# Kernel optimization log

Hardware: AMD Instinct MI355X
Metric: run time of the kernel (lower is better)

Reference implementation:

```python
import jax, jax.numpy as jnp
import numpy as np

N_NODES = 50000
N_EDGES = 400000
D_IN = 512
DIM_H = 256
N_GRAPHS = 64
BN_EPS = 1e-5


def _linear_init(key, din, dout):
    kw, kb = jax.random.split(key)
    s = 1.0 / np.sqrt(din)
    W = jax.random.uniform(kw, (din, dout), jnp.float32, -s, s)
    b = jax.random.uniform(kb, (dout,), jnp.float32, -s, s)
    return W, b


def setup_inputs() -> dict:
    key = jax.random.key(0)
    ks = iter(jax.random.split(key, 64))
    inp = {}
    inp["x"] = jax.random.normal(next(ks), (N_NODES, D_IN), jnp.float32)
    inp["edge_index"] = jax.random.randint(next(ks), (2, N_EDGES), 0, N_NODES, jnp.int32)
    inp["batch"] = jnp.sort(jax.random.randint(next(ks), (N_NODES,), 0, N_GRAPHS, jnp.int32))
    dins = [D_IN, DIM_H, DIM_H]
    for l in range(3):
        p = "c%d_" % (l + 1)
        inp[p + "W1"], inp[p + "b1"] = _linear_init(next(ks), dins[l], DIM_H)
        inp[p + "gamma"] = jax.random.uniform(next(ks), (DIM_H,), jnp.float32, 0.5, 1.5)
        inp[p + "beta"] = 0.1 * jax.random.normal(next(ks), (DIM_H,), jnp.float32)
        inp[p + "mean"] = 0.1 * jax.random.normal(next(ks), (DIM_H,), jnp.float32)
        inp[p + "var"] = jax.random.uniform(next(ks), (DIM_H,), jnp.float32, 0.5, 1.5)
        inp[p + "W2"], inp[p + "b2"] = _linear_init(next(ks), DIM_H, DIM_H)
    inp["lin1_W"], inp["lin1_b"] = _linear_init(next(ks), 3 * DIM_H, 64)
    inp["lin2_W"], inp["lin2_b"] = _linear_init(next(ks), 64, 2)
    return inp


def _gin_layer(x, src, dst, W1, b1, gamma, beta, mean, var, W2, b2):
    # GINConv with eps=0: h_i = MLP(x_i + sum_{j->i} x_j); scatter-add over edges
    agg = jax.ops.segment_sum(x[src], dst, num_segments=x.shape[0])
    h = (x + agg) @ W1 + b1
    # eval-mode BatchNorm1d
    h = jax.nn.relu((h - mean) * jax.lax.rsqrt(var + BN_EPS) * gamma + beta)
    return jax.nn.relu(h @ W2 + b2)


def reference(x, edge_index, batch,
              c1_W1, c1_b1, c1_gamma, c1_beta, c1_mean, c1_var, c1_W2, c1_b2,
              c2_W1, c2_b1, c2_gamma, c2_beta, c2_mean, c2_var, c2_W2, c2_b2,
              c3_W1, c3_b1, c3_gamma, c3_beta, c3_mean, c3_var, c3_W2, c3_b2,
              lin1_W, lin1_b, lin2_W, lin2_b):
    src, dst = edge_index[0], edge_index[1]
    h1 = _gin_layer(x, src, dst, c1_W1, c1_b1, c1_gamma, c1_beta, c1_mean, c1_var, c1_W2, c1_b2)
    h2 = _gin_layer(h1, src, dst, c2_W1, c2_b1, c2_gamma, c2_beta, c2_mean, c2_var, c2_W2, c2_b2)
    h3 = _gin_layer(h2, src, dst, c3_W1, c3_b1, c3_gamma, c3_beta, c3_mean, c3_var, c3_W2, c3_b2)
    # global_add_pool per graph
    p1 = jax.ops.segment_sum(h1, batch, num_segments=N_GRAPHS)
    p2 = jax.ops.segment_sum(h2, batch, num_segments=N_GRAPHS)
    p3 = jax.ops.segment_sum(h3, batch, num_segments=N_GRAPHS)
    h = jnp.concatenate([p1, p2, p3], axis=1)
    h = jax.nn.relu(h @ lin1_W + lin1_b)
    # Dropout(p=0.8) is identity in eval mode
    h = h @ lin2_W + lin2_b
    return (h, jax.nn.log_softmax(h, axis=1))
```

## Files before the change

kernel.cpp:

```cpp
#include <hip/hip_runtime.h>
#include <hip/hip_bf16.h>

#define DIV_UP(a,b) (((a)+(b)-1)/(b))

static const int NN  = 50000;
static const int NE  = 400000;
static const int DIN = 512;
static const int DH  = 256;
static const int NG  = 64;
static const int MAXDEG = 64;

typedef unsigned short u16;
typedef unsigned int   u32;
typedef __attribute__((ext_vector_type(8))) short bf16x8;
typedef __attribute__((ext_vector_type(4))) float f32x4;

#define AS1(p) ((const __attribute__((address_space(1))) void*)(p))
#define AS3(p) ((__attribute__((address_space(3))) void*)(p))

__device__ inline u16 f2bf(float f) {
  u32 u = __float_as_uint(f);
  u += 0x7fffu + ((u >> 16) & 1u);
  return (u16)(u >> 16);
}
__device__ inline float bf2f(u16 h) { return __uint_as_float(((u32)h) << 16); }
__device__ inline void unpack2(u32 u, float& lo, float& hi) {
  lo = __uint_as_float(u << 16);
  hi = __uint_as_float(u & 0xffff0000u);
}
__device__ inline u32 pack2(float lo, float hi) {
  return (u32)f2bf(lo) | ((u32)f2bf(hi) << 16);
}

struct SetupArgs {
  const float* Wsrc[6]; u16* Wdst[6];
  const float* bn[15];
  float* scsh;
  int* cnt; float* PL;
};
static const int NB_W = (131072 + 5 * 65536) / 256;
static const int NB_Z = DIV_UP(NN + NG * 768, 256);

__global__ __launch_bounds__(256) void k_setup(SetupArgs a) {
  int b = blockIdx.x;
  if (b < NB_W) {
    int idx = b * 256 + threadIdx.x;
    if (idx < 131072) {
      int n = idx >> 9, k = idx & 511;
      a.Wdst[0][idx] = f2bf(a.Wsrc[0][(size_t)k * 256 + n]);
    } else {
      int r = idx - 131072;
      int s = 1 + (r >> 16);
      int ri = r & 65535;
      int n = ri >> 8, k = ri & 255;
      a.Wdst[s][ri] = f2bf(a.Wsrc[s][(size_t)k * 256 + n]);
    }
  } else if (b < NB_W + 3) {
    int l = b - NB_W, ch = threadIdx.x;
    float sc = rsqrtf(a.bn[l * 5 + 4][ch] + 1e-5f) * a.bn[l * 5 + 1][ch];
    float sh = (a.bn[l * 5 + 0][ch] - a.bn[l * 5 + 3][ch]) * sc + a.bn[l * 5 + 2][ch];
    a.scsh[l * 512 + ch] = sc;
    a.scsh[l * 512 + 256 + ch] = sh;
  } else {
    int i = (b - NB_W - 3) * 256 + threadIdx.x;
    if (i < NN) a.cnt[i] = 0;
    else if (i - NN < NG * 768) a.PL[i - NN] = 0.f;
  }
}

__global__ __launch_bounds__(256) void k_fill2(const int* __restrict__ src,
                                               const int* __restrict__ dst,
                                               int* __restrict__ cnt,
                                               int* __restrict__ adj, int nE) {
  int e = blockIdx.x * 256 + threadIdx.x;
  if (e >= nE) return;
  int d = dst[e];
  int pos = atomicAdd(&cnt[d], 1);
  if (pos < MAXDEG) adj[(size_t)d * MAXDEG + pos] = src[e];
}

__global__ __launch_bounds__(256) void k_gather_bn(const u16* __restrict__ Y,
                                                   const int* __restrict__ cnt,
                                                   const int* __restrict__ adj,
                                                   const float* __restrict__ scsh,
                                                   u16* __restrict__ A) {
  int gid = blockIdx.x * 256 + threadIdx.x;
  int i = gid >> 5;
  if (i >= NN) return;
  int c = (gid & 31) << 3;
  uint4 v = *(const uint4*)(Y + (size_t)i * DH + c);
  float a0,a1,a2,a3,a4,a5,a6,a7;
  unpack2(v.x,a0,a1); unpack2(v.y,a2,a3); unpack2(v.z,a4,a5); unpack2(v.w,a6,a7);
  int deg = cnt[i]; if (deg > MAXDEG) deg = MAXDEG;
  const int* row = adj + (size_t)i * MAXDEG;
  int e = 0;
  for (; e + 8 <= deg; e += 8) {
    uint4 w[8];
#pragma unroll
    for (int u = 0; u < 8; ++u)
      w[u] = *(const uint4*)(Y + (size_t)row[e + u] * DH + c);
#pragma unroll
    for (int u = 0; u < 8; ++u) {
      float b0,b1,b2,b3,b4,b5,b6,b7;
      unpack2(w[u].x,b0,b1); unpack2(w[u].y,b2,b3);
      unpack2(w[u].z,b4,b5); unpack2(w[u].w,b6,b7);
      a0+=b0; a1+=b1; a2+=b2; a3+=b3; a4+=b4; a5+=b5; a6+=b6; a7+=b7;
    }
  }
  for (; e + 4 <= deg; e += 4) {
    uint4 w[4];
#pragma unroll
    for (int u = 0; u < 4; ++u)
      w[u] = *(const uint4*)(Y + (size_t)row[e + u] * DH + c);
#pragma unroll
    for (int u = 0; u < 4; ++u) {
      float b0,b1,b2,b3,b4,b5,b6,b7;
      unpack2(w[u].x,b0,b1); unpack2(w[u].y,b2,b3);
      unpack2(w[u].z,b4,b5); unpack2(w[u].w,b6,b7);
      a0+=b0; a1+=b1; a2+=b2; a3+=b3; a4+=b4; a5+=b5; a6+=b6; a7+=b7;
    }
  }
  for (; e < deg; ++e) {
    uint4 w = *(const uint4*)(Y + (size_t)row[e] * DH + c);
    float b0,b1,b2,b3,b4,b5,b6,b7;
    unpack2(w.x,b0,b1); unpack2(w.y,b2,b3); unpack2(w.z,b4,b5); unpack2(w.w,b6,b7);
    a0+=b0; a1+=b1; a2+=b2; a3+=b3; a4+=b4; a5+=b5; a6+=b6; a7+=b7;
  }
  float4 sc0 = *(const float4*)(scsh + c);
  float4 sc1 = *(const float4*)(scsh + c + 4);
  float4 sh0 = *(const float4*)(scsh + 256 + c);
  float4 sh1 = *(const float4*)(scsh + 256 + c + 4);
  a0 = fmaxf(fmaf(a0, sc0.x, sh0.x), 0.f);
  a1 = fmaxf(fmaf(a1, sc0.y, sh0.y), 0.f);
  a2 = fmaxf(fmaf(a2, sc0.z, sh0.z), 0.f);
  a3 = fmaxf(fmaf(a3, sc0.w, sh0.w), 0.f);
  a4 = fmaxf(fmaf(a4, sc1.x, sh1.x), 0.f);
  a5 = fmaxf(fmaf(a5, sc1.y, sh1.y), 0.f);
  a6 = fmaxf(fmaf(a6, sc1.z, sh1.z), 0.f);
  a7 = fmaxf(fmaf(a7, sc1.w, sh1.w), 0.f);
  uint4 o;
  o.x = pack2(a0,a1); o.y = pack2(a2,a3); o.z = pack2(a4,a5); o.w = pack2(a6,a7);
  *(uint4*)(A + (size_t)i * DH + c) = o;
}

template <int K, int F32A, int MODE, int POOL, int STORE>
__global__ __launch_bounds__(512, 4) void k_gemm(
    const u16* __restrict__ A, const float* __restrict__ A32,
    const u16* __restrict__ BT, const float* __restrict__ bias,
    u16* __restrict__ out, const int* __restrict__ batch,
    float* __restrict__ PL, int poolOff, int M) {
  const int N = 256;
  __shared__ __align__(16) u16 sm[32768];
  __shared__ int bsh[128];
  u16* Cs = sm;
  const int bm = blockIdx.x * 128;
  const int tid = threadIdx.x;
  const int lane = tid & 63;
  const int wave = tid >> 6;
  const int wm = (wave >> 2) * 64;
  const int wn = (wave & 3) * 64;
  const int l15 = lane & 15;
  const int l4 = lane >> 4;
  const int sw = (lane >> 1) & 3;
  const int srow = lane >> 2;
  const int sslot = (lane & 3) ^ ((lane >> 3) & 3);

  if (POOL && tid < 128) {
    int gm = bm + tid;
    bsh[tid] = (gm < M) ? batch[gm] : -1;
  }

  auto STAGE = [&](int buf, int k0) {
    u16* As = sm + buf * 12288;
    u16* Bs = As + 4096;
    {
      int row = wave * 16 + srow;
      int grA = bm + row; if (grA >= M) grA = M - 1;
      if (F32A) {
        const float* s = A32 + (size_t)grA * K + k0 + sslot * 8;
        float4 f0 = *(const float4*)s;
        float4 f1 = *(const float4*)(s + 4);
        uint4 o;
        o.x = pack2(f0.x, f0.y); o.y = pack2(f0.z, f0.w);
        o.z = pack2(f1.x, f1.y); o.w = pack2(f1.z, f1.w);
        *(uint4*)(As + row * 32 + (lane & 3) * 8) = o;
      } else {
        __builtin_amdgcn_global_load_lds(AS1(A + (size_t)grA * K + k0 + sslot * 8),
                                         AS3(As + wave * 512), 16, 0, 0);
      }
    }
#pragma unroll
    for (int i = 0; i < 2; ++i) {
      int q = wave * 2 + i;
      int row = q * 16 + srow;
      __builtin_amdgcn_global_load_lds(AS1(BT + (size_t)row * K + k0 + sslot * 8),
                                       AS3(Bs + q * 512), 16, 0, 0);
    }
  };

  f32x4 acc[4][4] = {};
  const int nt = K >> 5;
  STAGE(0, 0);
  int cur = 0;
  for (int t = 0; t < nt; ++t) {
    __syncthreads();
    if (t + 1 < nt) STAGE(cur ^ 1, (t + 1) << 5);
    u16* As = sm + cur * 12288;
    u16* Bs = As + 4096;
    bf16x8 af[4], bf_[4];
#pragma unroll
    for (int f = 0; f < 4; ++f) {
      af[f]  = *(const bf16x8*)(As + (wm + f * 16 + l15) * 32 + ((l4 ^ sw) << 3));
      bf_[f] = *(const bf16x8*)(Bs + (wn + f * 16 + l15) * 32 + ((l4 ^ sw) << 3));
    }
#pragma unroll
    for (int i = 0; i < 4; ++i)
#pragma unroll
      for (int j = 0; j < 4; ++j)
        acc[i][j] = __builtin_amdgcn_mfma_f32_16x16x32_bf16(af[i], bf_[j], acc[i][j], 0, 0, 0);
    cur ^= 1;
  }

  __syncthreads();
#pragma unroll
  for (int j = 0; j < 4; ++j) {
    int n = wn + j * 16 + l15;
    float sh = (MODE == 1) ? bias[n] : 0.f;
#pragma unroll
    for (int i = 0; i < 4; ++i) {
#pragma unroll
      for (int r = 0; r < 4; ++r) {
        int row = wm + i * 16 + l4 * 4 + r;
        float v = acc[i][j][r] + sh;
        if (MODE == 1) v = fmaxf(v, 0.f);
        Cs[row * 256 + n] = f2bf(v);
      }
    }
  }
  __syncthreads();

  if (STORE) {
    const int ccol = (tid & 31) * 8;
#pragma unroll
    for (int p = 0; p < 8; ++p) {
      int row = p * 16 + (tid >> 5);
      int gm = bm + row;
      if (gm < M)
        *(uint4*)(out + (size_t)gm * N + ccol) = *(const uint4*)(Cs + row * 256 + ccol);
    }
  }

  if (POOL) {
    int col = tid & 255;
    int half = tid >> 8;
    float accv = 0.f;
    int cg = bsh[half * 64];
    for (int r = 0; r < 64; ++r) {
      int row = half * 64 + r;
      int g = bsh[row];
      if (g != cg) {
        if (cg >= 0) unsafeAtomicAdd(&PL[cg * 768 + poolOff + col], accv);
        accv = 0.f;
        cg = g;
      }
      accv += bf2f(Cs[row * 256 + col]);
    }
    if (cg >= 0) unsafeAtomicAdd(&PL[cg * 768 + poolOff + col], accv);
  }
}

__global__ __launch_bounds__(64) void k_head1(const float* __restrict__ P,
                                              const float* __restrict__ W,
                                              const float* __restrict__ b,
                                              float* __restrict__ Q) {
  __shared__ float pr[768];
  int g = blockIdx.x, t = threadIdx.x;
  for (int i = t; i < 768; i += 64) pr[i] = P[g * 768 + i];
  __syncthreads();
  float acc = b[t];
  for (int k = 0; k < 768; ++k) acc = fmaf(pr[k], W[k * 64 + t], acc);
  Q[g * 64 + t] = fmaxf(acc, 0.f);
}

__global__ __launch_bounds__(64) void k_head2(const float* __restrict__ Q,
                                              const float* __restrict__ W,
                                              const float* __restrict__ b,
                                              float* __restrict__ out) {
  int g = threadIdx.x;
  if (g >= 64) return;
  float h0 = b[0], h1 = b[1];
  for (int k = 0; k < 64; ++k) {
    float q = Q[g * 64 + k];
    h0 = fmaf(q, W[k * 2 + 0], h0);
    h1 = fmaf(q, W[k * 2 + 1], h1);
  }
  out[g * 2 + 0] = h0;
  out[g * 2 + 1] = h1;
  float m = fmaxf(h0, h1);
  float lse = m + logf(expf(h0 - m) + expf(h1 - m));
  out[128 + g * 2 + 0] = h0 - lse;
  out[128 + g * 2 + 1] = h1 - lse;
}

extern "C" void kernel_launch(void* const* d_in, const int* in_sizes, int n_in,
                              void* d_out, int out_size, void* d_ws,
                              size_t ws_size, hipStream_t stream) {
  const float* x = (const float*)d_in[0];
  const int* ei = (const int*)d_in[1];
  const int* batch = (const int*)d_in[2];
  const float* W1[3]; const float* b1[3]; const float* ga[3]; const float* be[3];
  const float* mu[3]; const float* va[3]; const float* W2[3]; const float* b2[3];
  for (int l = 0; l < 3; ++l) {
    int base = 3 + 8 * l;
    W1[l] = (const float*)d_in[base + 0];
    b1[l] = (const float*)d_in[base + 1];
    ga[l] = (const float*)d_in[base + 2];
    be[l] = (const float*)d_in[base + 3];
    mu[l] = (const float*)d_in[base + 4];
    va[l] = (const float*)d_in[base + 5];
    W2[l] = (const float*)d_in[base + 6];
    b2[l] = (const float*)d_in[base + 7];
  }
  const float* l1W = (const float*)d_in[27];
  const float* l1b = (const float*)d_in[28];
  const float* l2W = (const float*)d_in[29];
  const float* l2b = (const float*)d_in[30];
  const int* src = ei;
  const int* dst = ei + NE;
  float* out = (float*)d_out;

  char* w = (char*)d_ws;
  u16* Yb  = (u16*)w; w += (size_t)NN * DH * 2;
  u16* Ab  = (u16*)w; w += (size_t)NN * DH * 2;
  u16* H1b = (u16*)w; w += (size_t)NN * DH * 2;
  u16* H2b = (u16*)w; w += (size_t)NN * DH * 2;
  u16* W1T[3]; u16* W2T[3];
  W1T[0] = (u16*)w; w += (size_t)DIN * DH * 2;
  for (int l = 1; l < 3; ++l) { W1T[l] = (u16*)w; w += (size_t)DH * DH * 2; }
  for (int l = 0; l < 3; ++l) { W2T[l] = (u16*)w; w += (size_t)DH * DH * 2; }
  float* scsh = (float*)w; w += 3 * 512 * 4;
  float* PL = (float*)w; w += NG * 768 * 4;
  float* Q  = (float*)w; w += NG * 64 * 4;
  int* cnt  = (int*)w; w += (size_t)NN * 4;
  int* adj  = (int*)w; w += (size_t)NN * MAXDEG * 4;

  SetupArgs sa;
  sa.Wsrc[0] = W1[0]; sa.Wdst[0] = W1T[0];
  sa.Wsrc[1] = W1[1]; sa.Wdst[1] = W1T[1];
  sa.Wsrc[2] = W1[2]; sa.Wdst[2] = W1T[2];
  for (int l = 0; l < 3; ++l) { sa.Wsrc[3 + l] = W2[l]; sa.Wdst[3 + l] = W2T[l]; }
  for (int l = 0; l < 3; ++l) {
    sa.bn[l * 5 + 0] = b1[l]; sa.bn[l * 5 + 1] = ga[l]; sa.bn[l * 5 + 2] = be[l];
    sa.bn[l * 5 + 3] = mu[l]; sa.bn[l * 5 + 4] = va[l];
  }
  sa.scsh = scsh; sa.cnt = cnt; sa.PL = PL;
  k_setup<<<NB_W + 3 + NB_Z, 256, 0, stream>>>(sa);

  k_fill2<<<DIV_UP(NE, 256), 256, 0, stream>>>(src, dst, cnt, adj, NE);

  const int g1 = DIV_UP(NN, 128);
  const int gg = DIV_UP(NN * 32, 256);
  const u16* hin[3] = {nullptr, H1b, H2b};
  u16* hout[3] = {H1b, H2b, H1b};

  for (int l = 0; l < 3; ++l) {
    if (l == 0)
      k_gemm<512, 1, 0, 0, 1><<<g1, 512, 0, stream>>>(nullptr, x, W1T[0], nullptr,
                                                      Yb, nullptr, nullptr, 0, NN);
    else
      k_gemm<256, 0, 0, 0, 1><<<g1, 512, 0, stream>>>(hin[l], nullptr, W1T[l], nullptr,
                                                      Yb, nullptr, nullptr, 0, NN);
    k_gather_bn<<<gg, 256, 0, stream>>>(Yb, cnt, adj, scsh + l * 512, Ab);
    if (l < 2)
      k_gemm<256, 0, 1, 1, 1><<<g1, 512, 0, stream>>>(Ab, nullptr, W2T[l], b2[l],
                                                      hout[l], batch, PL, 256 * l, NN);
    else
      k_gemm<256, 0, 1, 1, 0><<<g1, 512, 0, stream>>>(Ab, nullptr, W2T[l], b2[l],
                                                      hout[l], batch, PL, 256 * l, NN);
  }

  k_head1<<<NG, 64, 0, stream>>>(PL, l1W, l1b, Q);
  k_head2<<<1, 64, 0, stream>>>(Q, l2W, l2b, out);
}
```

Baseline: 267.9 us.

## Pad adjacency with zero sentinel row and gather two nodes per thread

Setup now fills the whole adjacency table with a sentinel index pointing to an extra all-zero row appended to Y. This lets the gather kernel round each degree up to a multiple of 8 and drop the remainder loops. Each thread now handles two nodes at once and issues 16 independent row loads per iteration, giving more memory-level parallelism. In exchange it does extra padded loads of the zero row, writes the full 12.8MB adjacency buffer during setup, and raises register pressure (launch bounds 256,3).

```diff
diff --git a/kernel.cpp b/kernel.cpp
--- a/kernel.cpp
+++ b/kernel.cpp
@@ -37,9 +37,11 @@
   const float* bn[15];
   float* scsh;
   int* cnt; float* PL;
+  int* adj; u16* Yb;
 };
 static const int NB_W = (131072 + 5 * 65536) / 256;
 static const int NB_Z = DIV_UP(NN + NG * 768, 256);
+static const int NB_A = (NN * MAXDEG / 4) / 256;
 
 __global__ __launch_bounds__(256) void k_setup(SetupArgs a) {
   int b = blockIdx.x;
@@ -61,10 +63,14 @@
     float sh = (a.bn[l * 5 + 0][ch] - a.bn[l * 5 + 3][ch]) * sc + a.bn[l * 5 + 2][ch];
     a.scsh[l * 512 + ch] = sc;
     a.scsh[l * 512 + 256 + ch] = sh;
-  } else {
+  } else if (b < NB_W + 3 + NB_Z) {
     int i = (b - NB_W - 3) * 256 + threadIdx.x;
     if (i < NN) a.cnt[i] = 0;
     else if (i - NN < NG * 768) a.PL[i - NN] = 0.f;
+  } else {
+    int idx = (b - NB_W - 3 - NB_Z) * 256 + threadIdx.x;
+    ((uint4*)a.adj)[idx] = make_uint4(NN, NN, NN, NN);
+    if (idx < 32) ((uint4*)(a.Yb + (size_t)NN * DH))[idx] = make_uint4(0, 0, 0, 0);
   }
 }
 
@@ -79,52 +85,49 @@
   if (pos < MAXDEG) adj[(size_t)d * MAXDEG + pos] = src[e];
 }
 
-__global__ __launch_bounds__(256) void k_gather_bn(const u16* __restrict__ Y,
-                                                   const int* __restrict__ cnt,
-                                                   const int* __restrict__ adj,
-                                                   const float* __restrict__ scsh,
-                                                   u16* __restrict__ A) {
+__global__ __launch_bounds__(256, 3) void k_gather_bn(const u16* __restrict__ Y,
+                                                      const int* __restrict__ cnt,
+                                                      const int* __restrict__ adj,
+                                                      const float* __restrict__ scsh,
+                                                      u16* __restrict__ A) {
   int gid = blockIdx.x * 256 + threadIdx.x;
-  int i = gid >> 5;
-  if (i >= NN) return;
-  int c = (gid & 31) << 3;
-  uint4 v = *(const uint4*)(Y + (size_t)i * DH + c);
-  float a0,a1,a2,a3,a4,a5,a6,a7;
-  unpack2(v.x,a0,a1); unpack2(v.y,a2,a3); unpack2(v.z,a4,a5); unpack2(v.w,a6,a7);
-  int deg = cnt[i]; if (deg > MAXDEG) deg = MAXDEG;
-  const int* row = adj + (size_t)i * MAXDEG;
-  int e = 0;
-  for (; e + 8 <= deg; e += 8) {
-    uint4 w[8];
+  int p = gid >> 5;
+  if (p >= NN / 2) return;
+  const int i0 = p * 2, i1 = p * 2 + 1;
+  const int c = (gid & 31) << 3;
+  float a0,a1,a2,a3,a4,a5,a6,a7v;
+  float b0,b1,b2,b3,b4,b5,b6,b7v;
+  uint4 v0 = *(const uint4*)(Y + (size_t)i0 * DH + c);
+  uint4 v1 = *(const uint4*)(Y + (size_t)i1 * DH + c);
+  unpack2(v0.x,a0,a1); unpack2(v0.y,a2,a3); unpack2(v0.z,a4,a5); unpack2(v0.w,a6,a7v);
+  unpack2(v1.x,b0,b1); unpack2(v1.y,b2,b3); unpack2(v1.z,b4,b5); unpack2(v1.w,b6,b7v);
+  int d0 = cnt[i0]; if (d0 > MAXDEG) d0 = MAXDEG; d0 = (d0 + 7) & ~7;
+  int d1 = cnt[i1]; if (d1 > MAXDEG) d1 = MAXDEG; d1 = (d1 + 7) & ~7;
+  const int* r0p = adj + (size_t)i0 * MAXDEG;
+  const int* r1p = adj + (size_t)i1 * MAXDEG;
+  int dm = d0 > d1 ? d0 : d1;
+  for (int e = 0; e < dm; e += 8) {
+    uint4 w0[8], w1[8];
 #pragma unroll
     for (int u = 0; u < 8; ++u)
-      w[u] = *(const uint4*)(Y + (size_t)row[e + u] * DH + c);
+      w0[u] = *(const uint4*)(Y + (size_t)r0p[e + u] * DH + c);
+#pragma unroll
+    for (int u = 0; u < 8; ++u)
+      w1[u] = *(const uint4*)(Y + (size_t)r1p[e + u] * DH + c);
 #pragma unroll
     for (int u = 0; u < 8; ++u) {
-      float b0,b1,b2,b3,b4,b5,b6,b7;
-      unpack2(w[u].x,b0,b1); unpack2(w[u].y,b2,b3);
-      unpack2(w[u].z,b4,b5); unpack2(w[u].w,b6,b7);
-      a0+=b0; a1+=b1; a2+=b2; a3+=b3; a4+=b4; a5+=b5; a6+=b6; a7+=b7;
-    }
-  }
-  for (; e + 4 <= deg; e += 4) {
-    uint4 w[4];
-#pragma unroll
-    for (int u = 0; u < 4; ++u)
-      w[u] = *(const uint4*)(Y + (size_t)row[e + u] * DH + c);
-#pragma unroll
-    for (int u = 0; u < 4; ++u) {
-      float b0,b1,b2,b3,b4,b5,b6,b7;
-      unpack2(w[u].x,b0,b1); unpack2(w[u].y,b2,b3);
-      unpack2(w[u].z,b4,b5); unpack2(w[u].w,b6,b7);
-      a0+=b0; a1+=b1; a2+=b2; a3+=b3; a4+=b4; a5+=b5; a6+=b6; a7+=b7;
-    }
-  }
-  for (; e < deg; ++e) {
-    uint4 w = *(const uint4*)(Y + (size_t)row[e] * DH + c);
-    float b0,b1,b2,b3,b4,b5,b6,b7;
-    unpack2(w.x,b0,b1); unpack2(w.y,b2,b3); unpack2(w.z,b4,b5); unpack2(w.w,b6,b7);
-    a0+=b0; a1+=b1; a2+=b2; a3+=b3; a4+=b4; a5+=b5; a6+=b6; a7+=b7;
+      float t0,t1,t2,t3,t4,t5,t6,t7;
+      unpack2(w0[u].x,t0,t1); unpack2(w0[u].y,t2,t3);
+      unpack2(w0[u].z,t4,t5); unpack2(w0[u].w,t6,t7);
+      a0+=t0; a1+=t1; a2+=t2; a3+=t3; a4+=t4; a5+=t5; a6+=t6; a7v+=t7;
+    }
+#pragma unroll
+    for (int u = 0; u < 8; ++u) {
+      float t0,t1,t2,t3,t4,t5,t6,t7;
+      unpack2(w1[u].x,t0,t1); unpack2(w1[u].y,t2,t3);
+      unpack2(w1[u].z,t4,t5); unpack2(w1[u].w,t6,t7);
+      b0+=t0; b1+=t1; b2+=t2; b3+=t3; b4+=t4; b5+=t5; b6+=t6; b7v+=t7;
+    }
   }
   float4 sc0 = *(const float4*)(scsh + c);
   float4 sc1 = *(const float4*)(scsh + c + 4);
@@ -137,10 +140,20 @@
   a4 = fmaxf(fmaf(a4, sc1.x, sh1.x), 0.f);
   a5 = fmaxf(fmaf(a5, sc1.y, sh1.y), 0.f);
   a6 = fmaxf(fmaf(a6, sc1.z, sh1.z), 0.f);
-  a7 = fmaxf(fmaf(a7, sc1.w, sh1.w), 0.f);
-  uint4 o;
-  o.x = pack2(a0,a1); o.y = pack2(a2,a3); o.z = pack2(a4,a5); o.w = pack2(a6,a7);
-  *(uint4*)(A + (size_t)i * DH + c) = o;
+  a7v = fmaxf(fmaf(a7v, sc1.w, sh1.w), 0.f);
+  b0 = fmaxf(fmaf(b0, sc0.x, sh0.x), 0.f);
+  b1 = fmaxf(fmaf(b1, sc0.y, sh0.y), 0.f);
+  b2 = fmaxf(fmaf(b2, sc0.z, sh0.z), 0.f);
+  b3 = fmaxf(fmaf(b3, sc0.w, sh0.w), 0.f);
+  b4 = fmaxf(fmaf(b4, sc1.x, sh1.x), 0.f);
+  b5 = fmaxf(fmaf(b5, sc1.y, sh1.y), 0.f);
+  b6 = fmaxf(fmaf(b6, sc1.z, sh1.z), 0.f);
+  b7v = fmaxf(fmaf(b7v, sc1.w, sh1.w), 0.f);
+  uint4 o0, o1;
+  o0.x = pack2(a0,a1); o0.y = pack2(a2,a3); o0.z = pack2(a4,a5); o0.w = pack2(a6,a7v);
+  o1.x = pack2(b0,b1); o1.y = pack2(b2,b3); o1.z = pack2(b4,b5); o1.w = pack2(b6,b7v);
+  *(uint4*)(A + (size_t)i0 * DH + c) = o0;
+  *(uint4*)(A + (size_t)i1 * DH + c) = o1;
 }
 
 template <int K, int F32A, int MODE, int POOL, int STORE>
@@ -330,7 +343,7 @@
   float* out = (float*)d_out;
 
   char* w = (char*)d_ws;
-  u16* Yb  = (u16*)w; w += (size_t)NN * DH * 2;
+  u16* Yb  = (u16*)w; w += (size_t)(NN + 1) * DH * 2;
   u16* Ab  = (u16*)w; w += (size_t)NN * DH * 2;
   u16* H1b = (u16*)w; w += (size_t)NN * DH * 2;
   u16* H2b = (u16*)w; w += (size_t)NN * DH * 2;
@@ -353,13 +366,13 @@
     sa.bn[l * 5 + 0] = b1[l]; sa.bn[l * 5 + 1] = ga[l]; sa.bn[l * 5 + 2] = be[l];
     sa.bn[l * 5 + 3] = mu[l]; sa.bn[l * 5 + 4] = va[l];
   }
-  sa.scsh = scsh; sa.cnt = cnt; sa.PL = PL;
-  k_setup<<<NB_W + 3 + NB_Z, 256, 0, stream>>>(sa);
+  sa.scsh = scsh; sa.cnt = cnt; sa.PL = PL; sa.adj = adj; sa.Yb = Yb;
+  k_setup<<<NB_W + 3 + NB_Z + NB_A, 256, 0, stream>>>(sa);
 
   k_fill2<<<DIV_UP(NE, 256), 256, 0, stream>>>(src, dst, cnt, adj, NE);
 
   const int g1 = DIV_UP(NN, 128);
-  const int gg = DIV_UP(NN * 32, 256);
+  const int gg = DIV_UP((NN / 2) * 32, 256);
   const u16* hin[3] = {nullptr, H1b, H2b};
   u16* hout[3] = {H1b, H2b, H1b};
 
```

Result: no change. 265.7 us (-0.8%).
